# Optimization experiments

Measured on AMD Instinct MI355X. Metric: run time of the kernel, lower is better.

Reference implementation:

```python
import jax, jax.numpy as jnp
import numpy as np

CUR, FULL, BS, D = 1024, 2048, 4, 1024
HN, HD = 16, 64
PREV = FULL - CUR
SCALE = 1.0 / HD ** 0.5


def rel_shift(x):
    # x: (bs, hn, cur, full) -> TXL relative shift over last two dims
    b, h, q, k = x.shape
    x = jnp.pad(x, ((0, 0), (0, 0), (0, 0), (1, 0)))  # (b,h,q,k+1)
    x = x.reshape(b, h, k + 1, q)[:, :, 1:, :]
    return x.reshape(b, h, q, k)


def setup_inputs() -> dict:
    key = jax.random.key(0)
    ks = jax.random.split(key, 16)
    s = 0.02
    inputs = jax.random.normal(ks[0], (CUR, BS, D), jnp.float32)
    pos_embedding = jax.random.normal(ks[1], (FULL, 1, D), jnp.float32)
    full_input = jax.random.normal(ks[2], (FULL, BS, D), jnp.float32)
    # causal mask: query i (absolute pos i+PREV) cannot attend to key j > i+PREV
    i = jnp.arange(CUR)[:, None]
    j = jnp.arange(FULL)[None, :]
    mask = (j > i + PREV)[:, :, None]  # (cur, full, 1) bool
    W_kv = jax.random.normal(ks[3], (D, 2 * HN * HD), jnp.float32) * s
    b_kv = jnp.zeros((2 * HN * HD,), jnp.float32)
    W_q = jax.random.normal(ks[4], (D, HN * HD), jnp.float32) * s
    b_q = jnp.zeros((HN * HD,), jnp.float32)
    W_pos = jax.random.normal(ks[5], (D, HN * HD), jnp.float32) * s
    b_pos = jnp.zeros((HN * HD,), jnp.float32)
    W_proj = jax.random.normal(ks[6], (HN * HD, D), jnp.float32) * s
    b_proj = jnp.zeros((D,), jnp.float32)
    u = jax.random.normal(ks[7], (HN, HD), jnp.float32) * s
    v = jax.random.normal(ks[8], (HN, HD), jnp.float32) * s
    return dict(inputs=inputs, pos_embedding=pos_embedding, full_input=full_input,
                u=u, v=v, mask=mask, W_kv=W_kv, b_kv=b_kv, W_q=W_q, b_q=b_q,
                W_pos=W_pos, b_pos=b_pos, W_proj=W_proj, b_proj=b_proj)


def reference(inputs, pos_embedding, full_input, u, v, mask,
              W_kv, b_kv, W_q, b_q, W_pos, b_pos, W_proj, b_proj):
    cur, bs, _ = inputs.shape
    full = full_input.shape[0]
    kv = full_input @ W_kv + b_kv                      # (full, bs, 2*hn*hd)
    k, val = jnp.split(kv, 2, axis=-1)
    k = k.reshape(full, bs, HN, HD)
    val = val.reshape(full, bs, HN, HD)
    q = (inputs @ W_q + b_q).reshape(cur, bs, HN, HD)
    r = (pos_embedding @ W_pos + b_pos).reshape(full, HN, HD)
    content = jnp.einsum('ibhd,jbhd->bhij', q + u, k)   # (bs,hn,cur,full)
    position = jnp.einsum('ibhd,jhd->bhij', q + v, r)
    position = rel_shift(position)
    attn = (content + position) * SCALE
    attn = jnp.where(mask[None, :, :, 0][:, None, :, :], -jnp.inf, attn)
    attn = jax.nn.softmax(attn, axis=-1)
    out = jnp.einsum('bhij,jbhd->ibhd', attn, val).reshape(cur, bs, HN * HD)
    return out @ W_proj + b_proj
```

## Files before the change

kernel.cpp:

```cpp
#include <hip/hip_runtime.h>


typedef _Float16 half8 __attribute__((ext_vector_type(8)));
typedef _Float16 half4v __attribute__((ext_vector_type(4)));
typedef float f32x4 __attribute__((ext_vector_type(4)));

typedef const __attribute__((address_space(1))) void* gas_ptr;
typedef __attribute__((address_space(3))) void* las_ptr;

__device__ __forceinline__ void load_lds16(const void* g, void* l) {
  __builtin_amdgcn_global_load_lds((gas_ptr)g, (las_ptr)l, 16, 0, 0);
}

__global__ __launch_bounds__(256) void prep(
    const float* __restrict__ inputs, const float* __restrict__ full_inp,
    const float* __restrict__ pos_emb, const float* __restrict__ Wq,
    const float* __restrict__ Wkv, const float* __restrict__ Wpos,
    const float* __restrict__ Wproj, _Float16* __restrict__ o_in,
    _Float16* __restrict__ o_full, _Float16* __restrict__ o_pos,
    _Float16* __restrict__ owq, _Float16* __restrict__ owkv,
    _Float16* __restrict__ owpos, _Float16* __restrict__ owproj) {
  __shared__ _Float16 tile[64][65];
  const int bx = blockIdx.x;
  const int t = threadIdx.x;
  if (bx < 14336) {
    size_t g = (size_t)bx * 256 + t;
    const float* src;
    _Float16* dst;
    size_t sg;
    if (g < (1u << 20)) {
      const int rd = (int)(g >> 8), b = rd >> 10, i = rd & 1023;
      src = inputs; dst = o_in;
      sg = ((size_t)(i * 4 + b) << 8) + (g & 255);
    } else if (g < (3u << 20)) {
      const size_t gd = g - (1u << 20);
      const int rd = (int)(gd >> 8), b = rd >> 11, j = rd & 2047;
      src = full_inp; dst = o_full;
      sg = ((size_t)(j * 4 + b) << 8) + (gd & 255);
      g = gd + (1u << 20);
      dst = o_full;
      sg = sg;
      float4 vv = *(const float4*)(src + sg * 4);
      half4v hh;
      hh[0] = (_Float16)vv.x; hh[1] = (_Float16)vv.y;
      hh[2] = (_Float16)vv.z; hh[3] = (_Float16)vv.w;
      *(half4v*)(dst + gd * 4) = hh;
      return;
    } else {
      const size_t gd = g - (3u << 20);
      float4 vv = *(const float4*)(pos_emb + gd * 4);
      half4v hh;
      hh[0] = (_Float16)vv.x; hh[1] = (_Float16)vv.y;
      hh[2] = (_Float16)vv.z; hh[3] = (_Float16)vv.w;
      *(half4v*)(o_pos + gd * 4) = hh;
      return;
    }
    float4 vv = *(const float4*)(src + sg * 4);
    half4v hh;
    hh[0] = (_Float16)vv.x; hh[1] = (_Float16)vv.y;
    hh[2] = (_Float16)vv.z; hh[3] = (_Float16)vv.w;
    *(half4v*)(dst + (g & ((1u << 20) - 1)) * 4) = hh;
    return;
  }
  const int wb = bx - 14336;
  const float* W;
  _Float16* Wt;
  int N, tidx;
  if (wb < 256) { W = Wq; Wt = owq; N = 1024; tidx = wb; }
  else if (wb < 768) { W = Wkv; Wt = owkv; N = 2048; tidx = wb - 256; }
  else if (wb < 1024) { W = Wpos; Wt = owpos; N = 1024; tidx = wb - 768; }
  else { W = Wproj; Wt = owproj; N = 1024; tidx = wb - 1024; }
  const int K = 1024;
  const int n0 = (tidx % (N >> 6)) * 64, k0 = (tidx / (N >> 6)) * 64;
  const int rr = t >> 2, cc = (t & 3) * 16;
#pragma unroll
  for (int i = 0; i < 4; ++i) {
    float4 v = *(const float4*)&W[(size_t)(k0 + rr) * N + n0 + cc + i * 4];
    tile[rr][cc + i * 4 + 0] = (_Float16)v.x;
    tile[rr][cc + i * 4 + 1] = (_Float16)v.y;
    tile[rr][cc + i * 4 + 2] = (_Float16)v.z;
    tile[rr][cc + i * 4 + 3] = (_Float16)v.w;
  }
  __syncthreads();
  const int n = t >> 2, kc = (t & 3) * 16;
#pragma unroll
  for (int i = 0; i < 4; ++i) {
    half4v h;
    h[0] = tile[kc + i * 4 + 0][n];
    h[1] = tile[kc + i * 4 + 1][n];
    h[2] = tile[kc + i * 4 + 2][n];
    h[3] = tile[kc + i * 4 + 3][n];
    *(half4v*)&Wt[(size_t)(n0 + n) * K + k0 + kc + i * 4] = h;
  }
}

__global__ __launch_bounds__(256, 2) void gemm3(
    const _Float16* __restrict__ Aq, const _Float16* __restrict__ Akv,
    const _Float16* __restrict__ Ar, const _Float16* __restrict__ Btq,
    const _Float16* __restrict__ Btkv, const _Float16* __restrict__ Btr,
    const float* __restrict__ bq, const float* __restrict__ bkv,
    const float* __restrict__ br, const float* __restrict__ uu,
    _Float16* __restrict__ qfu, _Float16* __restrict__ kf,
    _Float16* __restrict__ vfT, _Float16* __restrict__ rf) {
  __shared__ _Float16 smem[128 * 66];
  _Float16* As = smem;
  _Float16* Bs = smem + 4096;
  const int gb = blockIdx.x;
  const _Float16* A;
  const _Float16* Bt;
  const float* bias;
  int mode, bm, bn;
  if (gb < 256) {
    mode = 1; A = Aq; Bt = Btq; bias = bq;
    bn = (gb & 7) * 128; bm = (gb >> 3) * 128;
  } else if (gb < 1280) {
    mode = 2; A = Akv; Bt = Btkv; bias = bkv;
    const int j = gb - 256;
    bn = (j & 15) * 128; bm = (j >> 4) * 128;
  } else {
    mode = 3; A = Ar; Bt = Btr; bias = br;
    const int j = gb - 1280;
    bn = (j & 7) * 128; bm = (j >> 3) * 128;
  }
  const int K = 1024;
  const int t = threadIdx.x, w = t >> 6, l = t & 63;
  const int l15 = l & 15, l4 = l >> 4;
  const int wm = (w >> 1) * 64, wn = (w & 1) * 64;

  f32x4 acc[4][4];
  const f32x4 z4 = {0.f, 0.f, 0.f, 0.f};
#pragma unroll
  for (int i = 0; i < 4; ++i)
#pragma unroll
    for (int j = 0; j < 4; ++j) acc[i][j] = z4;

  const char* Abase = (const char*)A + (size_t)bm * K * 2;
  const char* Bbase = (const char*)Bt + (size_t)bn * K * 2;

  for (int k0 = 0; k0 < K; k0 += 32) {
    __syncthreads();
#pragma unroll
    for (int iss = 0; iss < 2; ++iss) {
      const int off = w * 1024 + iss * 4096 + l * 16;
      const int row = off >> 6, kb = off & 63;
      load_lds16(Abase + (size_t)row * (K * 2) + k0 * 2 + kb,
                 (char*)As + off);
      load_lds16(Bbase + (size_t)row * (K * 2) + k0 * 2 + kb,
                 (char*)Bs + off);
    }
    __syncthreads();
    half8 af[4], bf[4];
#pragma unroll
    for (int mt = 0; mt < 4; ++mt)
      af[mt] = *(const half8*)&As[(wm + mt * 16 + l15) * 32 + l4 * 8];
#pragma unroll
    for (int nt = 0; nt < 4; ++nt)
      bf[nt] = *(const half8*)&Bs[(wn + nt * 16 + l15) * 32 + l4 * 8];
#pragma unroll
    for (int mt = 0; mt < 4; ++mt)
#pragma unroll
      for (int nt = 0; nt < 4; ++nt)
        acc[mt][nt] = __builtin_amdgcn_mfma_f32_16x16x32_f16(
            af[mt], bf[nt], acc[mt][nt], 0, 0, 0);
  }

  if (mode == 2 && bn >= 1024) {
    const int b = bm >> 11, j0m = bm & 2047;
    const int hbase = (bn - 1024) >> 6;
#pragma unroll
    for (int ch = 0; ch < 2; ++ch) {
      __syncthreads();
      if (((wn >> 6) & 1) == ch) {
#pragma unroll
        for (int mt = 0; mt < 4; ++mt)
#pragma unroll
          for (int r = 0; r < 4; ++r) {
            const int rowl = wm + mt * 16 + l4 * 4 + r;
#pragma unroll
            for (int nt = 0; nt < 4; ++nt) {
              const int coll = nt * 16 + l15;
              smem[rowl * 66 + coll] =
                  (_Float16)(acc[mt][nt][r] + bias[bn + wn + coll]);
            }
          }
      }
      __syncthreads();
#pragma unroll
      for (int it = 0; it < 4; ++it) {
        const int c = t + 256 * it;
        const int d = c >> 4, ck = c & 15;
        half8 v8;
#pragma unroll
        for (int z = 0; z < 8; ++z) v8[z] = smem[(ck * 8 + z) * 66 + d];
        *(half8*)&vfT[(((size_t)(b * 16 + hbase + ch) * 64 + d) << 11) + j0m +
                      ck * 8] = v8;
      }
    }
    return;
  }

#pragma unroll
  for (int mt = 0; mt < 4; ++mt)
#pragma unroll
    for (int r = 0; r < 4; ++r) {
      const int rowl = wm + mt * 16 + l4 * 4 + r;
#pragma unroll
      for (int nt = 0; nt < 4; ++nt) {
        const int col = bn + wn + nt * 16 + l15;
        const float val = acc[mt][nt][r] + bias[col];
        if (mode == 1) {
          const int b = bm >> 10, i0m = bm & 1023;
          const int h = col >> 6, d = col & 63;
          qfu[(((size_t)(b * 16 + h) * 1024 + i0m + rowl) << 6) + d] =
              (_Float16)((val + uu[col]) * 0.125f);
        } else if (mode == 2) {
          const int b = bm >> 11, j0m = bm & 2047;
          const int h = col >> 6, d = col & 63;
          kf[(((size_t)(b * 16 + h) * 2048 + j0m + rowl) << 6) + d] =
              (_Float16)val;
        } else {
          const int h = col >> 6, d = col & 63;
          rf[(((size_t)h * 2048 + bm + rowl) << 6) + d] = (_Float16)val;
        }
      }
    }
}

__global__ __launch_bounds__(256, 2) void gemm_proj(
    const _Float16* __restrict__ A, const _Float16* __restrict__ Bt,
    const float* __restrict__ bias, float* __restrict__ out0, int M, int N,
    int K) {
  __shared__ _Float16 As[128 * 32];
  __shared__ _Float16 Bs[128 * 32];
  const int t = threadIdx.x, w = t >> 6, l = t & 63;
  const int l15 = l & 15, l4 = l >> 4;
  const int bm = blockIdx.y * 128, bn = blockIdx.x * 128;
  const int wm = (w >> 1) * 64, wn = (w & 1) * 64;

  f32x4 acc[4][4];
  const f32x4 z4 = {0.f, 0.f, 0.f, 0.f};
#pragma unroll
  for (int i = 0; i < 4; ++i)
#pragma unroll
    for (int j = 0; j < 4; ++j) acc[i][j] = z4;

  const char* Abase = (const char*)A + (size_t)bm * K * 2;
  const char* Bbase = (const char*)Bt + (size_t)bn * K * 2;

  for (int k0 = 0; k0 < K; k0 += 32) {
    __syncthreads();
#pragma unroll
    for (int iss = 0; iss < 2; ++iss) {
      const int off = w * 1024 + iss * 4096 + l * 16;
      const int row = off >> 6, kb = off & 63;
      load_lds16(Abase + (size_t)row * (K * 2) + k0 * 2 + kb,
                 (char*)As + off);
      load_lds16(Bbase + (size_t)row * (K * 2) + k0 * 2 + kb,
                 (char*)Bs + off);
    }
    __syncthreads();
    half8 af[4], bf[4];
#pragma unroll
    for (int mt = 0; mt < 4; ++mt)
      af[mt] = *(const half8*)&As[(wm + mt * 16 + l15) * 32 + l4 * 8];
#pragma unroll
    for (int nt = 0; nt < 4; ++nt)
      bf[nt] = *(const half8*)&Bs[(wn + nt * 16 + l15) * 32 + l4 * 8];
#pragma unroll
    for (int mt = 0; mt < 4; ++mt)
#pragma unroll
      for (int nt = 0; nt < 4; ++nt)
        acc[mt][nt] = __builtin_amdgcn_mfma_f32_16x16x32_f16(
            af[mt], bf[nt], acc[mt][nt], 0, 0, 0);
  }

#pragma unroll
  for (int mt = 0; mt < 4; ++mt)
#pragma unroll
    for (int r = 0; r < 4; ++r) {
      const int row = bm + wm + mt * 16 + l4 * 4 + r;
#pragma unroll
      for (int nt = 0; nt < 4; ++nt) {
        const int col = bn + wn + nt * 16 + l15;
        out0[(size_t)row * N + col] = acc[mt][nt][r] + bias[col];
      }
    }
}

__global__ __launch_bounds__(256, 2) void attn_mfma(
    const _Float16* __restrict__ qfu,
    const _Float16* __restrict__ kf,
    const _Float16* __restrict__ vfT,
    const _Float16* __restrict__ rf,
    const float* __restrict__ u,
    const float* __restrict__ v,
    _Float16* __restrict__ attn_out)
{
  __shared__ _Float16 ks[64 * 64];
  __shared__ _Float16 vts[64 * 64];
  __shared__ _Float16 rs[256 * 64];
  __shared__ _Float16 pA[4][16 * 64];

  const int t = threadIdx.x, w = t >> 6, l = t & 63;
  const int l15 = l & 15, l4 = l >> 4;
  const int id = blockIdx.x;
  const int bh = ((id >> 3) & 7) * 8 + (id & 7);
  const int bx = 15 - (id >> 6);
  const int i0 = bx * 64;
  const int h = bh & 15, b = bh >> 4;

  const char* kfb = (const char*)(kf + (((size_t)bh * 2048) << 6));
  const char* vg = (const char*)(vfT + (((size_t)bh) << 17));
  const char* rg = (const char*)(rf + (((size_t)h) << 17));

  half8 qa0, qa1, qv0, qv1;
  {
    const size_t qo = (((size_t)bh * 1024 + i0 + w * 16 + l15) << 6) + l4 * 8;
    qa0 = *(const half8*)(qfu + qo);
    qa1 = *(const half8*)(qfu + qo + 32);
    half8 dl0, dl1;
#pragma unroll
    for (int z = 0; z < 8; ++z) {
      const int di = l4 * 8 + z;
      dl0[z] = (_Float16)(0.125f * (v[h * 64 + di] - u[h * 64 + di]));
      dl1[z] = (_Float16)(0.125f * (v[h * 64 + 32 + di] - u[h * 64 + 32 + di]));
    }
    qv0 = qa0 + dl0;
    qv1 = qa1 + dl1;
  }
  const f32x4 z4 = {0.f, 0.f, 0.f, 0.f};
  f32x4 o[4];
  o[0] = z4; o[1] = z4; o[2] = z4; o[3] = z4;
  float lsum[4] = {0.f, 0.f, 0.f, 0.f};

  const int mb0 = 960 - i0;
  const int njt = bx + 17;

#pragma unroll
  for (int iss = 0; iss < 4; ++iss) {
    const int off = w * 1024 + iss * 4096 + l * 16;
    const int q = off >> 7;
    const int cph = (off >> 4) & 7;
    const int slot = (mb0 + q) & 255;
    int m = mb0 + q;
    m = m < 2047 ? m : 2047;
    load_lds16(rg + (size_t)m * 128 + ((cph ^ (slot & 7)) << 4),
               (char*)rs + slot * 128 + cph * 16);
  }

  for (int jt = 0; jt < njt; ++jt) {
    const int j0 = jt * 64;
    const int m_base = j0 - i0 + 960;
    __syncthreads();
    {
      const char* kg = kfb + (size_t)j0 * 128;
#pragma unroll
      for (int iss = 0; iss < 2; ++iss) {
        const int off = w * 1024 + iss * 4096 + l * 16;
        const int row = off >> 7;
        const int cph = (off >> 4) & 7;
        const int sw = ((cph ^ (row & 7)) << 4);
        load_lds16(kg + (size_t)row * 128 + sw, (char*)ks + off);
        load_lds16(vg + (size_t)row * 4096 + (size_t)j0 * 2 + sw,
                   (char*)vts + off);
      }
    }
    if (jt > 0) {
      const int m0 = m_base + 64;
#pragma unroll
      for (int iss = 0; iss < 2; ++iss) {
        const int off = w * 1024 + iss * 4096 + l * 16;
        const int q = off >> 7;
        const int cph = (off >> 4) & 7;
        const int slot = (m0 + q) & 255;
        int m = m0 + q;
        m = m < 2047 ? m : 2047;
        load_lds16(rg + (size_t)m * 128 + ((cph ^ (slot & 7)) << 4),
                   (char*)rs + slot * 128 + cph * 16);
      }
    }
    __syncthreads();

    f32x4 sc[4];
#pragma unroll
    for (int nt = 0; nt < 4; ++nt) {
      const int row = nt * 16 + l15;
      const int rsw = row & 7;
      const half8 b0 = *(const half8*)&ks[row * 64 + ((l4 ^ rsw) * 8)];
      const half8 b1 = *(const half8*)&ks[row * 64 + (((4 + l4) ^ rsw) * 8)];
      f32x4 cc = z4;
      cc = __builtin_amdgcn_mfma_f32_16x16x32_f16(qa0, b0, cc, 0, 0, 0);
      cc = __builtin_amdgcn_mfma_f32_16x16x32_f16(qa1, b1, cc, 0, 0, 0);
      sc[nt] = cc;
    }
    f32x4 accP[5];
#pragma unroll
    for (int p = 0; p < 5; ++p) {
      const int m = m_base + (3 - w + p) * 16 + l15;
      const int slot = m & 255;
      const int ssw = slot & 7;
      const half8 b0 = *(const half8*)&rs[slot * 64 + ((l4 ^ ssw) * 8)];
      const half8 b1 = *(const half8*)&rs[slot * 64 + (((4 + l4) ^ ssw) * 8)];
      f32x4 cc = z4;
      cc = __builtin_amdgcn_mfma_f32_16x16x32_f16(qv0, b0, cc, 0, 0, 0);
      cc = __builtin_amdgcn_mfma_f32_16x16x32_f16(qv1, b1, cc, 0, 0, 0);
      accP[p] = cc;
    }

    const int cw = i0 - j0 + 1024 + 16 * w;
    if (cw >= 63) {
#pragma unroll
      for (int r = 0; r < 4; ++r) {
        const int thr = 4 * l4 + r;
        const int srcl = (l4 << 4) | ((15 + l15 - thr) & 15);
        float rot[5];
#pragma unroll
        for (int p = 0; p < 5; ++p) rot[p] = __shfl(accP[p][r], srcl, 64);
        float esum = 0.f;
        const int sw2 = (thr & 7) * 8;
#pragma unroll
        for (int nt = 0; nt < 4; ++nt) {
          const float pv = (l15 <= thr) ? rot[nt] : rot[nt + 1];
          const float e = __expf(sc[nt][r] + pv);
          esum += e;
          pA[w][thr * 64 + ((16 * nt + l15) ^ sw2)] = (_Float16)e;
        }
        lsum[r] += esum;
      }
    } else {
#pragma unroll
      for (int r = 0; r < 4; ++r) {
        const int thr = 4 * l4 + r;
        const int srcl = (l4 << 4) | ((15 + l15 - thr) & 15);
        float rot[5];
#pragma unroll
        for (int p = 0; p < 5; ++p) rot[p] = __shfl(accP[p][r], srcl, 64);
        float esum = 0.f;
        const int sw2 = (thr & 7) * 8;
#pragma unroll
        for (int nt = 0; nt < 4; ++nt) {
          const float pv = (l15 <= thr) ? rot[nt] : rot[nt + 1];
          const bool masked = (16 * nt + l15) > (cw + thr);
          const float e = masked ? 0.f : __expf(sc[nt][r] + pv);
          esum += e;
          pA[w][thr * 64 + ((16 * nt + l15) ^ sw2)] = (_Float16)e;
        }
        lsum[r] += esum;
      }
    }
#pragma unroll
    for (int kk = 0; kk < 2; ++kk) {
      const half8 a8 = *(const half8*)&pA[w][l15 * 64 + ((kk * 32 + l4 * 8) ^
                                                        ((l15 & 7) * 8))];
#pragma unroll
      for (int nt = 0; nt < 4; ++nt) {
        const int row = nt * 16 + l15;
        const half8 b8 =
            *(const half8*)&vts[row * 64 + ((((kk << 2) + l4) ^ (row & 7)) * 8)];
        o[nt] = __builtin_amdgcn_mfma_f32_16x16x32_f16(a8, b8, o[nt], 0, 0, 0);
      }
    }
  }

#pragma unroll
  for (int r = 0; r < 4; ++r) {
    float s = lsum[r];
    s += __shfl_xor(s, 1, 64);
    s += __shfl_xor(s, 2, 64);
    s += __shfl_xor(s, 4, 64);
    s += __shfl_xor(s, 8, 64);
    const float inv = 1.0f / s;
    const int i = i0 + w * 16 + l4 * 4 + r;
    const size_t base = ((size_t)i * 4 + b) * 1024 + h * 64;
#pragma unroll
    for (int nt = 0; nt < 4; ++nt)
      attn_out[base + nt * 16 + l15] = (_Float16)(o[nt][r] * inv);
  }
}

extern "C" void kernel_launch(void* const* d_in, const int* in_sizes, int n_in,
                              void* d_out, int out_size, void* d_ws,
                              size_t ws_size, hipStream_t stream) {
  const float* inputs   = (const float*)d_in[0];
  const float* pos_emb  = (const float*)d_in[1];
  const float* full_inp = (const float*)d_in[2];
  const float* u        = (const float*)d_in[3];
  const float* v        = (const float*)d_in[4];
  const float* W_kv   = (const float*)d_in[6];
  const float* b_kv   = (const float*)d_in[7];
  const float* W_q    = (const float*)d_in[8];
  const float* b_q    = (const float*)d_in[9];
  const float* W_pos  = (const float*)d_in[10];
  const float* b_pos  = (const float*)d_in[11];
  const float* W_proj = (const float*)d_in[12];
  const float* b_proj = (const float*)d_in[13];
  float* out = (float*)d_out;

  char* ws = (char*)d_ws;
  const size_t MB = 1024 * 1024;
  _Float16* in_q_h    = (_Float16*)(ws);
  _Float16* in_full_h = (_Float16*)(ws + 8 * MB);
  _Float16* in_pos_h  = (_Float16*)(ws + 24 * MB);
  _Float16* attn_h    = (_Float16*)(ws + 28 * MB);
  _Float16* wq_t      = (_Float16*)(ws + 36 * MB);
  _Float16* wkv_t     = (_Float16*)(ws + 38 * MB);
  _Float16* wpos_t    = (_Float16*)(ws + 42 * MB);
  _Float16* wproj_t   = (_Float16*)(ws + 44 * MB);
  _Float16* qfu       = (_Float16*)(ws + 46 * MB);
  _Float16* kf        = (_Float16*)(ws + 54 * MB);
  _Float16* vfT       = (_Float16*)(ws + 70 * MB);
  _Float16* rf        = (_Float16*)(ws + 86 * MB);

  const dim3 blk(256);
  prep<<<dim3(15616), blk, 0, stream>>>(inputs, full_inp, pos_emb, W_q, W_kv,
                                        W_pos, W_proj, in_q_h, in_full_h,
                                        in_pos_h, wq_t, wkv_t, wpos_t, wproj_t);
  gemm3<<<dim3(1408), blk, 0, stream>>>(in_q_h, in_full_h, in_pos_h, wq_t,
                                        wkv_t, wpos_t, b_q, b_kv, b_pos, u,
                                        qfu, kf, vfT, rf);
  attn_mfma<<<dim3(1024), blk, 0, stream>>>(qfu, kf, vfT, rf, u, v, attn_h);
  gemm_proj<<<dim3(8, 32), blk, 0, stream>>>(attn_h, wproj_t, b_proj, out,
                                             4096, 1024, 1024);
}
```

Baseline: 334.1 us.

## Load positional R fragments directly from global instead of an LDS ring buffer

Drops the 32 KB shared-memory ring buffer for the positional embedding R and its async global-to-LDS prefetch. Each wave now reads its R fragments straight from global memory into registers every tile. Launch bounds are raised from 2 to 4 blocks per SM to use the freed LDS for occupancy. The trade-off is more global/L2 traffic with redundant reads across waves, global load latency sitting right before the MFMAs, and a tighter register budget at higher occupancy.

```diff
diff --git a/kernel.cpp b/kernel.cpp
--- a/kernel.cpp
+++ b/kernel.cpp
@@ -37,9 +37,6 @@
       const int rd = (int)(gd >> 8), b = rd >> 11, j = rd & 2047;
       src = full_inp; dst = o_full;
       sg = ((size_t)(j * 4 + b) << 8) + (gd & 255);
-      g = gd + (1u << 20);
-      dst = o_full;
-      sg = sg;
       float4 vv = *(const float4*)(src + sg * 4);
       half4v hh;
       hh[0] = (_Float16)vv.x; hh[1] = (_Float16)vv.y;
@@ -287,7 +284,7 @@
     }
 }
 
-__global__ __launch_bounds__(256, 2) void attn_mfma(
+__global__ __launch_bounds__(256, 4) void attn_mfma(
     const _Float16* __restrict__ qfu,
     const _Float16* __restrict__ kf,
     const _Float16* __restrict__ vfT,
@@ -298,7 +295,6 @@
 {
   __shared__ _Float16 ks[64 * 64];
   __shared__ _Float16 vts[64 * 64];
-  __shared__ _Float16 rs[256 * 64];
   __shared__ _Float16 pA[4][16 * 64];
 
   const int t = threadIdx.x, w = t >> 6, l = t & 63;
@@ -333,20 +329,7 @@
   o[0] = z4; o[1] = z4; o[2] = z4; o[3] = z4;
   float lsum[4] = {0.f, 0.f, 0.f, 0.f};
 
-  const int mb0 = 960 - i0;
   const int njt = bx + 17;
-
-#pragma unroll
-  for (int iss = 0; iss < 4; ++iss) {
-    const int off = w * 1024 + iss * 4096 + l * 16;
-    const int q = off >> 7;
-    const int cph = (off >> 4) & 7;
-    const int slot = (mb0 + q) & 255;
-    int m = mb0 + q;
-    m = m < 2047 ? m : 2047;
-    load_lds16(rg + (size_t)m * 128 + ((cph ^ (slot & 7)) << 4),
-               (char*)rs + slot * 128 + cph * 16);
-  }
 
   for (int jt = 0; jt < njt; ++jt) {
     const int j0 = jt * 64;
@@ -365,21 +348,17 @@
                    (char*)vts + off);
       }
     }
-    if (jt > 0) {
-      const int m0 = m_base + 64;
-#pragma unroll
-      for (int iss = 0; iss < 2; ++iss) {
-        const int off = w * 1024 + iss * 4096 + l * 16;
-        const int q = off >> 7;
-        const int cph = (off >> 4) & 7;
-        const int slot = (m0 + q) & 255;
-        int m = m0 + q;
-        m = m < 2047 ? m : 2047;
-        load_lds16(rg + (size_t)m * 128 + ((cph ^ (slot & 7)) << 4),
-                   (char*)rs + slot * 128 + cph * 16);
-      }
-    }
-    __syncthreads();
+    __syncthreads();
+
+    half8 rb[5][2];
+#pragma unroll
+    for (int p = 0; p < 5; ++p) {
+      int m = m_base + (3 - w + p) * 16 + l15;
+      m = m < 2047 ? m : 2047;
+      const half8* rrow = (const half8*)(rg + (size_t)m * 128);
+      rb[p][0] = rrow[l4];
+      rb[p][1] = rrow[4 + l4];
+    }
 
     f32x4 sc[4];
 #pragma unroll
@@ -396,14 +375,9 @@
     f32x4 accP[5];
 #pragma unroll
     for (int p = 0; p < 5; ++p) {
-      const int m = m_base + (3 - w + p) * 16 + l15;
-      const int slot = m & 255;
-      const int ssw = slot & 7;
-      const half8 b0 = *(const half8*)&rs[slot * 64 + ((l4 ^ ssw) * 8)];
-      const half8 b1 = *(const half8*)&rs[slot * 64 + (((4 + l4) ^ ssw) * 8)];
       f32x4 cc = z4;
-      cc = __builtin_amdgcn_mfma_f32_16x16x32_f16(qv0, b0, cc, 0, 0, 0);
-      cc = __builtin_amdgcn_mfma_f32_16x16x32_f16(qv1, b1, cc, 0, 0, 0);
+      cc = __builtin_amdgcn_mfma_f32_16x16x32_f16(qv0, rb[p][0], cc, 0, 0, 0);
+      cc = __builtin_amdgcn_mfma_f32_16x16x32_f16(qv1, rb[p][1], cc, 0, 0, 0);
       accP[p] = cc;
     }
 
```

Result: slower. 389.2 us (+16.5%).

## Double-buffer K/V tiles and prefetch next tile in attention loop

Applied to the files above, without the earlier changes.

The attention kernel now keeps two LDS buffers each for the K and V^T tiles. It issues the asynchronous global-to-LDS loads for tile jt+1, plus the matching relative-position rows, before computing on tile jt. The first tile is loaded before the loop, and the two barriers per iteration become one at the end. The goal is to overlap global memory latency with MFMA work, at the cost of 16KB more LDS per block, which may pressure occupancy at two blocks per CU. Redundant dead assignments in the prep kernel are also removed.

```diff
diff --git a/kernel.cpp b/kernel.cpp
--- a/kernel.cpp
+++ b/kernel.cpp
@@ -37,9 +37,6 @@
       const int rd = (int)(gd >> 8), b = rd >> 11, j = rd & 2047;
       src = full_inp; dst = o_full;
       sg = ((size_t)(j * 4 + b) << 8) + (gd & 255);
-      g = gd + (1u << 20);
-      dst = o_full;
-      sg = sg;
       float4 vv = *(const float4*)(src + sg * 4);
       half4v hh;
       hh[0] = (_Float16)vv.x; hh[1] = (_Float16)vv.y;
@@ -296,8 +293,8 @@
     const float* __restrict__ v,
     _Float16* __restrict__ attn_out)
 {
-  __shared__ _Float16 ks[64 * 64];
-  __shared__ _Float16 vts[64 * 64];
+  __shared__ _Float16 ks[2][64 * 64];
+  __shared__ _Float16 vts[2][64 * 64];
   __shared__ _Float16 rs[256 * 64];
   __shared__ _Float16 pA[4][16 * 64];
 
@@ -336,6 +333,17 @@
   const int mb0 = 960 - i0;
   const int njt = bx + 17;
 
+  {
+#pragma unroll
+    for (int iss = 0; iss < 2; ++iss) {
+      const int off = w * 1024 + iss * 4096 + l * 16;
+      const int row = off >> 7;
+      const int cph = (off >> 4) & 7;
+      const int sw = ((cph ^ (row & 7)) << 4);
+      load_lds16(kfb + (size_t)row * 128 + sw, (char*)ks[0] + off);
+      load_lds16(vg + (size_t)row * 4096 + sw, (char*)vts[0] + off);
+    }
+  }
 #pragma unroll
   for (int iss = 0; iss < 4; ++iss) {
     const int off = w * 1024 + iss * 4096 + l * 16;
@@ -347,26 +355,26 @@
     load_lds16(rg + (size_t)m * 128 + ((cph ^ (slot & 7)) << 4),
                (char*)rs + slot * 128 + cph * 16);
   }
-
+  __syncthreads();
+
+  int cur = 0;
   for (int jt = 0; jt < njt; ++jt) {
     const int j0 = jt * 64;
     const int m_base = j0 - i0 + 960;
-    __syncthreads();
-    {
-      const char* kg = kfb + (size_t)j0 * 128;
+
+    if (jt + 1 < njt) {
+      const char* kg = kfb + (size_t)(j0 + 64) * 128;
 #pragma unroll
       for (int iss = 0; iss < 2; ++iss) {
         const int off = w * 1024 + iss * 4096 + l * 16;
         const int row = off >> 7;
         const int cph = (off >> 4) & 7;
         const int sw = ((cph ^ (row & 7)) << 4);
-        load_lds16(kg + (size_t)row * 128 + sw, (char*)ks + off);
-        load_lds16(vg + (size_t)row * 4096 + (size_t)j0 * 2 + sw,
-                   (char*)vts + off);
-      }
-    }
-    if (jt > 0) {
-      const int m0 = m_base + 64;
+        load_lds16(kg + (size_t)row * 128 + sw, (char*)ks[cur ^ 1] + off);
+        load_lds16(vg + (size_t)row * 4096 + (size_t)(j0 + 64) * 2 + sw,
+                   (char*)vts[cur ^ 1] + off);
+      }
+      const int m0 = m_base + 128;
 #pragma unroll
       for (int iss = 0; iss < 2; ++iss) {
         const int off = w * 1024 + iss * 4096 + l * 16;
@@ -379,15 +387,17 @@
                    (char*)rs + slot * 128 + cph * 16);
       }
     }
-    __syncthreads();
+
+    const _Float16* ksc = ks[cur];
+    const _Float16* vtsc = vts[cur];
 
     f32x4 sc[4];
 #pragma unroll
     for (int nt = 0; nt < 4; ++nt) {
       const int row = nt * 16 + l15;
       const int rsw = row & 7;
-      const half8 b0 = *(const half8*)&ks[row * 64 + ((l4 ^ rsw) * 8)];
-      const half8 b1 = *(const half8*)&ks[row * 64 + (((4 + l4) ^ rsw) * 8)];
+      const half8 b0 = *(const half8*)&ksc[row * 64 + ((l4 ^ rsw) * 8)];
+      const half8 b1 = *(const half8*)&ksc[row * 64 + (((4 + l4) ^ rsw) * 8)];
       f32x4 cc = z4;
       cc = __builtin_amdgcn_mfma_f32_16x16x32_f16(qa0, b0, cc, 0, 0, 0);
       cc = __builtin_amdgcn_mfma_f32_16x16x32_f16(qa1, b1, cc, 0, 0, 0);
@@ -455,11 +465,14 @@
 #pragma unroll
       for (int nt = 0; nt < 4; ++nt) {
         const int row = nt * 16 + l15;
-        const half8 b8 =
-            *(const half8*)&vts[row * 64 + ((((kk << 2) + l4) ^ (row & 7)) * 8)];
+        const half8 b8 = *(const half8*)&vtsc[row * 64 +
+                                             ((((kk << 2) + l4) ^ (row & 7)) * 8)];
         o[nt] = __builtin_amdgcn_mfma_f32_16x16x32_f16(a8, b8, o[nt], 0, 0, 0);
       }
     }
+
+    __syncthreads();
+    cur ^= 1;
   }
 
 #pragma unroll
```

New measurement: 328.0 us. No clear change (-1.8%).

## Process two 64-row query tiles per attention block to reuse K/V/R tiles

Applied to the files above, without the earlier changes.

The attention kernel now handles 128 query rows per block, as two 64-row groups sharing each loaded K, V^T and positional tile, which halves the grid to 512 blocks. The positional ring-buffer prefetch is widened to cover the extra group, and the first group skips work on fully masked tiles. Block ordering interleaves heavy and light query tiles to balance load. This cuts global/LDS traffic per query, at the cost of more registers and LDS (double pA) and fewer blocks to spread across CUs.

```diff
diff --git a/kernel.cpp b/kernel.cpp
--- a/kernel.cpp
+++ b/kernel.cpp
@@ -37,9 +37,6 @@
       const int rd = (int)(gd >> 8), b = rd >> 11, j = rd & 2047;
       src = full_inp; dst = o_full;
       sg = ((size_t)(j * 4 + b) << 8) + (gd & 255);
-      g = gd + (1u << 20);
-      dst = o_full;
-      sg = sg;
       float4 vv = *(const float4*)(src + sg * 4);
       half4v hh;
       hh[0] = (_Float16)vv.x; hh[1] = (_Float16)vv.y;
@@ -299,25 +296,23 @@
   __shared__ _Float16 ks[64 * 64];
   __shared__ _Float16 vts[64 * 64];
   __shared__ _Float16 rs[256 * 64];
-  __shared__ _Float16 pA[4][16 * 64];
+  __shared__ _Float16 pA[2][4][16 * 64];
 
   const int t = threadIdx.x, w = t >> 6, l = t & 63;
   const int l15 = l & 15, l4 = l >> 4;
   const int id = blockIdx.x;
   const int bh = ((id >> 3) & 7) * 8 + (id & 7);
-  const int bx = 15 - (id >> 6);
-  const int i0 = bx * 64;
+  const int qt = id >> 6;
+  const int bx = (qt < 4) ? (7 - qt) : (qt - 4);
+  const int i0 = bx * 128;
   const int h = bh & 15, b = bh >> 4;
 
   const char* kfb = (const char*)(kf + (((size_t)bh * 2048) << 6));
   const char* vg = (const char*)(vfT + (((size_t)bh) << 17));
   const char* rg = (const char*)(rf + (((size_t)h) << 17));
 
-  half8 qa0, qa1, qv0, qv1;
+  half8 qa0[2], qa1[2], qv0[2], qv1[2];
   {
-    const size_t qo = (((size_t)bh * 1024 + i0 + w * 16 + l15) << 6) + l4 * 8;
-    qa0 = *(const half8*)(qfu + qo);
-    qa1 = *(const half8*)(qfu + qo + 32);
     half8 dl0, dl1;
 #pragma unroll
     for (int z = 0; z < 8; ++z) {
@@ -325,24 +320,34 @@
       dl0[z] = (_Float16)(0.125f * (v[h * 64 + di] - u[h * 64 + di]));
       dl1[z] = (_Float16)(0.125f * (v[h * 64 + 32 + di] - u[h * 64 + 32 + di]));
     }
-    qv0 = qa0 + dl0;
-    qv1 = qa1 + dl1;
+#pragma unroll
+    for (int g = 0; g < 2; ++g) {
+      const size_t qo =
+          (((size_t)bh * 1024 + i0 + 64 * g + w * 16 + l15) << 6) + l4 * 8;
+      qa0[g] = *(const half8*)(qfu + qo);
+      qa1[g] = *(const half8*)(qfu + qo + 32);
+      qv0[g] = qa0[g] + dl0;
+      qv1[g] = qa1[g] + dl1;
+    }
   }
   const f32x4 z4 = {0.f, 0.f, 0.f, 0.f};
-  f32x4 o[4];
-  o[0] = z4; o[1] = z4; o[2] = z4; o[3] = z4;
-  float lsum[4] = {0.f, 0.f, 0.f, 0.f};
+  f32x4 o[2][4];
+  float lsum[2][4];
+#pragma unroll
+  for (int g = 0; g < 2; ++g)
+#pragma unroll
+    for (int nt = 0; nt < 4; ++nt) { o[g][nt] = z4; lsum[g][nt] = 0.f; }
 
   const int mb0 = 960 - i0;
-  const int njt = bx + 17;
-
-#pragma unroll
-  for (int iss = 0; iss < 4; ++iss) {
+  const int njt = 2 * bx + 18;
+
+#pragma unroll
+  for (int iss = 0; iss < 6; ++iss) {
     const int off = w * 1024 + iss * 4096 + l * 16;
     const int q = off >> 7;
     const int cph = (off >> 4) & 7;
-    const int slot = (mb0 + q) & 255;
-    int m = mb0 + q;
+    const int slot = (mb0 - 64 + q) & 255;
+    int m = mb0 - 64 + q;
     m = m < 2047 ? m : 2047;
     load_lds16(rg + (size_t)m * 128 + ((cph ^ (slot & 7)) << 4),
                (char*)rs + slot * 128 + cph * 16);
@@ -381,101 +386,119 @@
     }
     __syncthreads();
 
-    f32x4 sc[4];
+    f32x4 sc[2][4];
 #pragma unroll
     for (int nt = 0; nt < 4; ++nt) {
       const int row = nt * 16 + l15;
       const int rsw = row & 7;
       const half8 b0 = *(const half8*)&ks[row * 64 + ((l4 ^ rsw) * 8)];
       const half8 b1 = *(const half8*)&ks[row * 64 + (((4 + l4) ^ rsw) * 8)];
-      f32x4 cc = z4;
-      cc = __builtin_amdgcn_mfma_f32_16x16x32_f16(qa0, b0, cc, 0, 0, 0);
-      cc = __builtin_amdgcn_mfma_f32_16x16x32_f16(qa1, b1, cc, 0, 0, 0);
-      sc[nt] = cc;
-    }
-    f32x4 accP[5];
-#pragma unroll
-    for (int p = 0; p < 5; ++p) {
-      const int m = m_base + (3 - w + p) * 16 + l15;
-      const int slot = m & 255;
-      const int ssw = slot & 7;
-      const half8 b0 = *(const half8*)&rs[slot * 64 + ((l4 ^ ssw) * 8)];
-      const half8 b1 = *(const half8*)&rs[slot * 64 + (((4 + l4) ^ ssw) * 8)];
-      f32x4 cc = z4;
-      cc = __builtin_amdgcn_mfma_f32_16x16x32_f16(qv0, b0, cc, 0, 0, 0);
-      cc = __builtin_amdgcn_mfma_f32_16x16x32_f16(qv1, b1, cc, 0, 0, 0);
-      accP[p] = cc;
-    }
-
-    const int cw = i0 - j0 + 1024 + 16 * w;
-    if (cw >= 63) {
-#pragma unroll
-      for (int r = 0; r < 4; ++r) {
-        const int thr = 4 * l4 + r;
-        const int srcl = (l4 << 4) | ((15 + l15 - thr) & 15);
-        float rot[5];
-#pragma unroll
-        for (int p = 0; p < 5; ++p) rot[p] = __shfl(accP[p][r], srcl, 64);
-        float esum = 0.f;
-        const int sw2 = (thr & 7) * 8;
-#pragma unroll
-        for (int nt = 0; nt < 4; ++nt) {
-          const float pv = (l15 <= thr) ? rot[nt] : rot[nt + 1];
-          const float e = __expf(sc[nt][r] + pv);
-          esum += e;
-          pA[w][thr * 64 + ((16 * nt + l15) ^ sw2)] = (_Float16)e;
+#pragma unroll
+      for (int g = 0; g < 2; ++g) {
+        f32x4 cc = z4;
+        cc = __builtin_amdgcn_mfma_f32_16x16x32_f16(qa0[g], b0, cc, 0, 0, 0);
+        cc = __builtin_amdgcn_mfma_f32_16x16x32_f16(qa1[g], b1, cc, 0, 0, 0);
+        sc[g][nt] = cc;
+      }
+    }
+
+#pragma unroll
+    for (int g = 0; g < 2; ++g) {
+      const int cw = i0 + 64 * g - j0 + 1024 + 16 * w;
+      if (g == 0 && cw < -15) continue;
+      const int mbg = m_base - 64 * g;
+      f32x4 accP[5];
+#pragma unroll
+      for (int p = 0; p < 5; ++p) {
+        const int m = mbg + (3 - w + p) * 16 + l15;
+        const int slot = m & 255;
+        const int ssw = slot & 7;
+        const half8 b0 = *(const half8*)&rs[slot * 64 + ((l4 ^ ssw) * 8)];
+        const half8 b1 = *(const half8*)&rs[slot * 64 + (((4 + l4) ^ ssw) * 8)];
+        f32x4 cc = z4;
+        cc = __builtin_amdgcn_mfma_f32_16x16x32_f16(qv0[g], b0, cc, 0, 0, 0);
+        cc = __builtin_amdgcn_mfma_f32_16x16x32_f16(qv1[g], b1, cc, 0, 0, 0);
+        accP[p] = cc;
+      }
+      if (cw >= 63) {
+#pragma unroll
+        for (int r = 0; r < 4; ++r) {
+          const int thr = 4 * l4 + r;
+          const int srcl = (l4 << 4) | ((15 + l15 - thr) & 15);
+          float rot[5];
+#pragma unroll
+          for (int p = 0; p < 5; ++p) rot[p] = __shfl(accP[p][r], srcl, 64);
+          float esum = 0.f;
+          const int sw2 = (thr & 7) * 8;
+#pragma unroll
+          for (int nt = 0; nt < 4; ++nt) {
+            const float pv = (l15 <= thr) ? rot[nt] : rot[nt + 1];
+            const float e = __expf(sc[g][nt][r] + pv);
+            esum += e;
+            pA[g][w][thr * 64 + ((16 * nt + l15) ^ sw2)] = (_Float16)e;
+          }
+          lsum[g][r] += esum;
         }
-        lsum[r] += esum;
-      }
-    } else {
-#pragma unroll
-      for (int r = 0; r < 4; ++r) {
-        const int thr = 4 * l4 + r;
-        const int srcl = (l4 << 4) | ((15 + l15 - thr) & 15);
-        float rot[5];
-#pragma unroll
-        for (int p = 0; p < 5; ++p) rot[p] = __shfl(accP[p][r], srcl, 64);
-        float esum = 0.f;
-        const int sw2 = (thr & 7) * 8;
-#pragma unroll
-        for (int nt = 0; nt < 4; ++nt) {
-          const float pv = (l15 <= thr) ? rot[nt] : rot[nt + 1];
-          const bool masked = (16 * nt + l15) > (cw + thr);
-          const float e = masked ? 0.f : __expf(sc[nt][r] + pv);
-          esum += e;
-          pA[w][thr * 64 + ((16 * nt + l15) ^ sw2)] = (_Float16)e;
+      } else {
+#pragma unroll
+        for (int r = 0; r < 4; ++r) {
+          const int thr = 4 * l4 + r;
+          const int srcl = (l4 << 4) | ((15 + l15 - thr) & 15);
+          float rot[5];
+#pragma unroll
+          for (int p = 0; p < 5; ++p) rot[p] = __shfl(accP[p][r], srcl, 64);
+          float esum = 0.f;
+          const int sw2 = (thr & 7) * 8;
+#pragma unroll
+          for (int nt = 0; nt < 4; ++nt) {
+            const float pv = (l15 <= thr) ? rot[nt] : rot[nt + 1];
+            const bool masked = (16 * nt + l15) > (cw + thr);
+            const float e = masked ? 0.f : __expf(sc[g][nt][r] + pv);
+            esum += e;
+            pA[g][w][thr * 64 + ((16 * nt + l15) ^ sw2)] = (_Float16)e;
+          }
+          lsum[g][r] += esum;
         }
-        lsum[r] += esum;
-      }
-    }
+      }
+    }
+
+    const bool act0 = (i0 - j0 + 1024 + 16 * w) >= -15;
 #pragma unroll
     for (int kk = 0; kk < 2; ++kk) {
-      const half8 a8 = *(const half8*)&pA[w][l15 * 64 + ((kk * 32 + l4 * 8) ^
-                                                        ((l15 & 7) * 8))];
+      const int aoff = l15 * 64 + ((kk * 32 + l4 * 8) ^ ((l15 & 7) * 8));
+      half8 a81 = *(const half8*)&pA[1][w][aoff];
+      half8 a80;
+      if (act0) a80 = *(const half8*)&pA[0][w][aoff];
 #pragma unroll
       for (int nt = 0; nt < 4; ++nt) {
         const int row = nt * 16 + l15;
         const half8 b8 =
             *(const half8*)&vts[row * 64 + ((((kk << 2) + l4) ^ (row & 7)) * 8)];
-        o[nt] = __builtin_amdgcn_mfma_f32_16x16x32_f16(a8, b8, o[nt], 0, 0, 0);
-      }
-    }
-  }
-
-#pragma unroll
-  for (int r = 0; r < 4; ++r) {
-    float s = lsum[r];
-    s += __shfl_xor(s, 1, 64);
-    s += __shfl_xor(s, 2, 64);
-    s += __shfl_xor(s, 4, 64);
-    s += __shfl_xor(s, 8, 64);
-    const float inv = 1.0f / s;
-    const int i = i0 + w * 16 + l4 * 4 + r;
-    const size_t base = ((size_t)i * 4 + b) * 1024 + h * 64;
-#pragma unroll
-    for (int nt = 0; nt < 4; ++nt)
-      attn_out[base + nt * 16 + l15] = (_Float16)(o[nt][r] * inv);
-  }
+        if (act0)
+          o[0][nt] =
+              __builtin_amdgcn_mfma_f32_16x16x32_f16(a80, b8, o[0][nt], 0, 0, 0);
+        o[1][nt] =
+            __builtin_amdgcn_mfma_f32_16x16x32_f16(a81, b8, o[1][nt], 0, 0, 0);
+      }
+    }
+  }
+
+#pragma unroll
+  for (int g = 0; g < 2; ++g)
+#pragma unroll
+    for (int r = 0; r < 4; ++r) {
+      float s = lsum[g][r];
+      s += __shfl_xor(s, 1, 64);
+      s += __shfl_xor(s, 2, 64);
+      s += __shfl_xor(s, 4, 64);
+      s += __shfl_xor(s, 8, 64);
+      const float inv = 1.0f / s;
+      const int i = i0 + 64 * g + w * 16 + l4 * 4 + r;
+      const size_t base = ((size_t)i * 4 + b) * 1024 + h * 64;
+#pragma unroll
+      for (int nt = 0; nt < 4; ++nt)
+        attn_out[base + nt * 16 + l15] = (_Float16)(o[g][nt][r] * inv);
+    }
 }
 
 extern "C" void kernel_launch(void* const* d_in, const int* in_sizes, int n_in,
@@ -518,7 +541,7 @@
   gemm3<<<dim3(1408), blk, 0, stream>>>(in_q_h, in_full_h, in_pos_h, wq_t,
                                         wkv_t, wpos_t, b_q, b_kv, b_pos, u,
                                         qfu, kf, vfT, rf);
-  attn_mfma<<<dim3(1024), blk, 0, stream>>>(qfu, kf, vfT, rf, u, v, attn_h);
+  attn_mfma<<<dim3(512), blk, 0, stream>>>(qfu, kf, vfT, rf, u, v, attn_h);
   gemm_proj<<<dim3(8, 32), blk, 0, stream>>>(attn_h, wproj_t, b_proj, out,
                                              4096, 1024, 1024);
 }
```

Measured after the change: 333.1 us. About the same (-0.3%).
